# Kernel tuning notes

Measured on AMD Instinct MI355X. Metric: run time of the kernel, lower is better.

Reference implementation:

```python
import jax, jax.numpy as jnp
import numpy as np

N_QUBITS = 8
DEPTH = 3


def _apply_1q(state, U, q):
    # state: (2,)*n complex, apply 2x2 unitary U on qubit axis q
    state = jnp.moveaxis(state, q, -1)
    state = state @ U.T
    return jnp.moveaxis(state, -1, q)


def _ry(state, theta, q):
    h = theta * 0.5
    c, s = jnp.cos(h), jnp.sin(h)
    U = jnp.stack([jnp.stack([c, -s]), jnp.stack([s, c])]).astype(jnp.complex64)
    return _apply_1q(state, U, q)


def _rz(state, theta, q):
    h = theta * 0.5
    d = jnp.stack([jnp.exp(-1j * h), jnp.exp(1j * h)]).astype(jnp.complex64)
    state = jnp.moveaxis(state, q, -1) * d
    return jnp.moveaxis(state, -1, q)


def _cx(state, c, t):
    # CNOT with control c, target t: flip target amplitudes where control=1
    state = jnp.moveaxis(state, (c, t), (-2, -1))
    s0 = state[..., 0, :]
    s1 = state[..., 1, ::-1]
    state = jnp.stack([s0, s1], axis=-2)
    return jnp.moveaxis(state, (-2, -1), (c, t))


def _simulate(angles, qparams):
    # Single-sample circuit: RY angle encoding, then DEPTH layers of (RZ,RY) per
    # qubit + CX ring. Returns <Z_0> (Hamiltonian 'Z' + 'I'*(n-1)).
    state = jnp.zeros((2,) * N_QUBITS, jnp.complex64).at[(0,) * N_QUBITS].set(1.0)
    for q in range(N_QUBITS):
        state = _ry(state, angles[q], q)
    idx = 0
    for _ in range(DEPTH):
        for q in range(N_QUBITS):
            state = _rz(state, qparams[idx], q); idx += 1
            state = _ry(state, qparams[idx], q); idx += 1
        for i in range(N_QUBITS):
            state = _cx(state, i, (i + 1) % N_QUBITS)
    probs = jnp.abs(state) ** 2
    return probs[0].sum() - probs[1].sum()


def setup_inputs() -> dict:
    key = jax.random.key(0)
    ks = jax.random.split(key, 6)
    B, F, H = 16384, 16, 256
    nq = 2 * N_QUBITS * DEPTH  # 48 variational params
    return {
        "x": jax.random.normal(ks[0], (B, F), jnp.float32),
        "enc_w1": jax.random.normal(ks[1], (H, F), jnp.float32) / np.sqrt(F).astype(np.float32),
        "enc_b1": jnp.zeros((H,), jnp.float32),
        "enc_w2": jax.random.normal(ks[2], (N_QUBITS, H), jnp.float32) / np.sqrt(H).astype(np.float32),
        "enc_b2": jnp.zeros((N_QUBITS,), jnp.float32),
        "qparams": jax.random.normal(ks[3], (nq,), jnp.float32) * 0.1,
        "dec_w1": jax.random.normal(ks[4], (H, 1), jnp.float32),
        "dec_b1": jnp.zeros((H,), jnp.float32),
        "dec_w2": jax.random.normal(ks[5], (1, H), jnp.float32) / np.sqrt(H).astype(np.float32),
        "dec_b2": jnp.zeros((1,), jnp.float32),
    }


def reference(x, enc_w1, enc_b1, enc_w2, enc_b2, qparams, dec_w1, dec_b1, dec_w2, dec_b2):
    # encoder: Linear -> ReLU -> Linear -> Tanh, scaled by pi (angle encoding)
    h = jax.nn.relu(x @ enc_w1.T + enc_b1)
    angles = jnp.tanh(h @ enc_w2.T + enc_b2) * jnp.pi  # (B, n_qubits)
    # vectorized quantum state-vector simulation over the batch
    expvals = jax.vmap(_simulate, in_axes=(0, None))(angles, qparams)  # (B,)
    q = expvals[:, None]  # (B, 1)
    # decoder: Linear(1->H) -> ReLU -> Linear(H->1) -> Sigmoid
    d = jax.nn.relu(q @ dec_w1.T + dec_b1)
    return jax.nn.sigmoid(d @ dec_w2.T + dec_b2)
```

## Files before the change

### kernel.cpp

```cpp
#include <hip/hip_runtime.h>
#include <math.h>

#define NQ 8
#define DEPTH 3
#define FDIM 16
#define HDIM 256
#define WAVES_PER_BLOCK 4
#define THREADS (WAVES_PER_BLOCK * 64)
#define NGATE (NQ * DEPTH)
#define PI_F 3.14159265358979323846f

template<int CTRL>
__device__ __forceinline__ float dpp1(float v) {
    return __int_as_float(__builtin_amdgcn_update_dpp(
        0, __float_as_int(v), CTRL, 0xF, 0xF, true));
}

template<int M4>
__device__ __forceinline__ float shuf4(float v) {
    if constexpr (M4 == 0)  return v;
    else if constexpr (M4 == 1)  return dpp1<0xB1>(v);
    else if constexpr (M4 == 2)  return dpp1<0x4E>(v);
    else if constexpr (M4 == 3)  return dpp1<0x1B>(v);
    else if constexpr (M4 == 4)  return dpp1<0x1B>(dpp1<0x141>(v));
    else if constexpr (M4 == 5)  return dpp1<0x4E>(dpp1<0x141>(v));
    else if constexpr (M4 == 6)  return dpp1<0xB1>(dpp1<0x141>(v));
    else if constexpr (M4 == 7)  return dpp1<0x141>(v);
    else if constexpr (M4 == 8)  return dpp1<0x128>(v);
    else if constexpr (M4 == 9)  return dpp1<0xB1>(dpp1<0x128>(v));
    else if constexpr (M4 == 10) return dpp1<0x4E>(dpp1<0x128>(v));
    else if constexpr (M4 == 11) return dpp1<0x1B>(dpp1<0x128>(v));
    else if constexpr (M4 == 12) return dpp1<0x1B>(dpp1<0x140>(v));
    else if constexpr (M4 == 13) return dpp1<0x4E>(dpp1<0x140>(v));
    else if constexpr (M4 == 14) return dpp1<0xB1>(dpp1<0x140>(v));
    else                         return dpp1<0x140>(v);
}

template<int ML>
__device__ __forceinline__ float shuf(float v, int lane) {
    if constexpr (ML == 0) {
        return v;
    } else if constexpr (ML >= 32) {
        int addr = (lane ^ ML) << 2;
        return __int_as_float(__builtin_amdgcn_ds_bpermute(addr, __float_as_int(v)));
    } else if constexpr (ML >= 16) {
        return __int_as_float(__builtin_amdgcn_ds_swizzle(
            __float_as_int(v), (ML << 10) | 0x1F));
    } else {
        return shuf4<ML>(v);
    }
}

__device__ __forceinline__ float px16(float v, int lane) {
#if __has_builtin(__builtin_amdgcn_permlane16_swap)
    auto r = __builtin_amdgcn_permlane16_swap(__float_as_int(v), __float_as_int(v), false, false);
    return __int_as_float((lane & 16) ? r[0] : r[1]);
#else
    return __shfl_xor(v, 16, 64);
#endif
}
__device__ __forceinline__ float px32(float v, int lane) {
#if __has_builtin(__builtin_amdgcn_permlane32_swap)
    auto r = __builtin_amdgcn_permlane32_swap(__float_as_int(v), __float_as_int(v), false, false);
    return __int_as_float((lane & 32) ? r[0] : r[1]);
#else
    return __shfl_xor(v, 32, 64);
#endif
}

__device__ __forceinline__ float wred(float v, int lane) {
    v += shuf4<1>(v);
    v += shuf4<2>(v);
    v += shuf4<4>(v);
    v += shuf4<8>(v);
    v += px16(v, lane);
    v += px32(v, lane);
    return v;
}

__device__ __forceinline__ float fast_tanh(float y) {
    float ex = __expf(2.f * y);
    return 1.f - 2.f * __builtin_amdgcn_rcpf(ex + 1.f);
}

template<int M, int R>
__device__ __forceinline__ void gate2(float (&sr)[4], float (&si)[4],
                                      float cz, float szv, float cy, float sy,
                                      int lane) {
    constexpr int ML = M & 63, MH = (M >> 6) & 3;
    constexpr int RL = R & 63, RH = (R >> 6) & 3;
    bool p0;
    if constexpr (RL == 0)                 p0 = false;
    else if constexpr ((RL & (RL-1)) == 0) p0 = (lane & RL) != 0;
    else                                   p0 = (__popc(lane & RL) & 1) != 0;
    float sgz = p0 ? szv : -szv;
    float sgy = p0 ? sy  : -sy;
#pragma unroll
    for (int hi = 0; hi < 4; hi++) {
        const bool f = (__builtin_popcount(hi & RH) & 1) != 0;
        float z = f ? -sgz : sgz;
        float nr = fmaf(sr[hi], cz, -(si[hi] * z));
        float ni = fmaf(si[hi], cz,  (sr[hi] * z));
        sr[hi] = nr; si[hi] = ni;
    }
    float pr[4], pi[4];
#pragma unroll
    for (int hi = 0; hi < 4; hi++) {
        pr[hi] = shuf<ML>(sr[hi ^ MH], lane);
        pi[hi] = shuf<ML>(si[hi ^ MH], lane);
    }
#pragma unroll
    for (int hi = 0; hi < 4; hi++) {
        const bool f = (__builtin_popcount(hi & RH) & 1) != 0;
        float yv = f ? -sgy : sgy;
        sr[hi] = fmaf(yv, pr[hi], cy * sr[hi]);
        si[hi] = fmaf(yv, pi[hi], cy * si[hi]);
    }
}

__global__ __launch_bounds__(THREADS) void hqcl_kernel(
    const float* __restrict__ x,
    const float* __restrict__ w1,
    const float* __restrict__ b1,
    const float* __restrict__ w2,
    const float* __restrict__ b2,
    const float* __restrict__ qp,
    const float* __restrict__ dw1,
    const float* __restrict__ db1,
    const float* __restrict__ dw2,
    const float* __restrict__ db2,
    float* __restrict__ out, int B)
{
    __shared__ float4 sG4[NGATE];

    const int t = threadIdx.x;
    if (t < 2 * NGATE) {
        float s, c;
        __sincosf(qp[t] * 0.5f, &s, &c);
        float* p = (float*)&sG4[t >> 1] + 2 * (t & 1);
        p[0] = c; p[1] = s;
    }
    __syncthreads();

    const int lane = t & 63;
    const int row  = blockIdx.x * WAVES_PER_BLOCK + (t >> 6);
    if (row >= B) return;

    const float4* xp = (const float4*)(x + row * FDIM);
    float4 x0 = xp[0], x1 = xp[1], x2 = xp[2], x3 = xp[3];

    float hreg[4];
#pragma unroll
    for (int m = 0; m < 4; m++) {
        int j = lane + 64 * m;
        const float4* wp = (const float4*)(w1 + j * FDIM);
        float4 wa = wp[0], wb = wp[1], wc = wp[2], wd = wp[3];
        float acc = b1[j];
        acc = fmaf(x0.x, wa.x, acc); acc = fmaf(x0.y, wa.y, acc);
        acc = fmaf(x0.z, wa.z, acc); acc = fmaf(x0.w, wa.w, acc);
        acc = fmaf(x1.x, wb.x, acc); acc = fmaf(x1.y, wb.y, acc);
        acc = fmaf(x1.z, wb.z, acc); acc = fmaf(x1.w, wb.w, acc);
        acc = fmaf(x2.x, wc.x, acc); acc = fmaf(x2.y, wc.y, acc);
        acc = fmaf(x2.z, wc.z, acc); acc = fmaf(x2.w, wc.w, acc);
        acc = fmaf(x3.x, wd.x, acc); acc = fmaf(x3.y, wd.y, acc);
        acc = fmaf(x3.z, wd.z, acc); acc = fmaf(x3.w, wd.w, acc);
        hreg[m] = fmaxf(acc, 0.f);
    }

    float c0[NQ], s0[NQ];
#pragma unroll
    for (int q = 0; q < NQ; q++) {
        float a = 0.f;
#pragma unroll
        for (int m = 0; m < 4; m++)
            a = fmaf(hreg[m], w2[q * HDIM + lane + 64 * m], a);
        a = wred(a, lane);
        float ang = fast_tanh(a + b2[q]) * PI_F;
        __sincosf(ang * 0.5f, &s0[q], &c0[q]);
    }

    float pl = 1.f;
#pragma unroll
    for (int b = 0; b < 6; b++) {
        int q = 7 - b;
        pl *= ((lane >> b) & 1) ? s0[q] : c0[q];
    }
    float sr[4], si[4];
    sr[0] = pl * c0[1] * c0[0];
    sr[1] = pl * s0[1] * c0[0];
    sr[2] = pl * c0[1] * s0[0];
    sr[3] = pl * s0[1] * s0[0];
#pragma unroll
    for (int hi = 0; hi < 4; hi++) si[hi] = 0.f;

#define GATE(L, Q, MM, RR) { float4 g4 = sG4[(L)*8 + (Q)]; \
        gate2<MM, RR>(sr, si, g4.x, g4.y, g4.z, g4.w, lane); }
    GATE(0,0,0x80,0x80) GATE(0,1,0x40,0x40) GATE(0,2,0x20,0x20) GATE(0,3,0x10,0x10)
    GATE(0,4,0x08,0x08) GATE(0,5,0x04,0x04) GATE(0,6,0x02,0x02) GATE(0,7,0x01,0x01)
    GATE(1,0,0xC0,0x7F) GATE(1,1,0x60,0xC0) GATE(1,2,0x30,0xE0) GATE(1,3,0x18,0xF0)
    GATE(1,4,0x0C,0xF8) GATE(1,5,0x06,0xFC) GATE(1,6,0x03,0xFE) GATE(1,7,0xC1,0xFF)
    GATE(2,0,0xA0,0xD5) GATE(2,1,0x50,0xBF) GATE(2,2,0x28,0x5F) GATE(2,3,0x14,0xAF)
    GATE(2,4,0x0A,0x57) GATE(2,5,0x05,0xAB) GATE(2,6,0xC2,0x55) GATE(2,7,0x61,0xAA)
#undef GATE

    float m0 = sr[0]*sr[0] + si[0]*si[0] + sr[2]*sr[2] + si[2]*si[2];
    float m1 = sr[1]*sr[1] + si[1]*si[1] + sr[3]*sr[3] + si[3]*si[3];
    bool pb = (__popc(lane & 0x0C) & 1) != 0;
    float e = pb ? (m1 - m0) : (m0 - m1);
    e = wred(e, lane);

    float acc = 0.f;
#pragma unroll
    for (int m = 0; m < 4; m++) {
        int j = lane + 64 * m;
        float d = fmaxf(fmaf(e, dw1[j], db1[j]), 0.f);
        acc = fmaf(d, dw2[j], acc);
    }
    acc = wred(acc, lane);
    if (lane == 0) out[row] = 1.f / (1.f + __expf(-(acc + db2[0])));
}

extern "C" void kernel_launch(void* const* d_in, const int* in_sizes, int n_in,
                              void* d_out, int out_size, void* d_ws, size_t ws_size,
                              hipStream_t stream) {
    const float* x   = (const float*)d_in[0];
    const float* w1  = (const float*)d_in[1];
    const float* b1  = (const float*)d_in[2];
    const float* w2  = (const float*)d_in[3];
    const float* b2  = (const float*)d_in[4];
    const float* qp  = (const float*)d_in[5];
    const float* dw1 = (const float*)d_in[6];
    const float* db1 = (const float*)d_in[7];
    const float* dw2 = (const float*)d_in[8];
    const float* db2 = (const float*)d_in[9];
    float* out = (float*)d_out;

    const int B = in_sizes[0] / FDIM;
    const int grid = (B + WAVES_PER_BLOCK - 1) / WAVES_PER_BLOCK;
    hqcl_kernel<<<grid, THREADS, 0, stream>>>(x, w1, b1, w2, b2, qp, dw1, db1, dw2, db2, out, B);
}
```

Baseline: 42.86 us.

## Simulate four samples per wave with 16-lane state groups and fused RZ·RY gates

Each wave now handles four batch rows. The encoder still runs per row in a loop, and the angles go through LDS. The quantum simulation then packs four samples into one wave, 16 lanes each with 16 amplitudes per lane, so all lane shuffles are cheap DPP ops instead of ds_swizzle/bpermute. The RZ and RY gates are precombined into one fused 2x2 complex update using products of their sin/cos, and the decoder runs four rows at once. The cost is higher register pressure (32 state floats), a serial encoder loop, and an extra block barrier.

```diff
diff --git a/kernel.cpp b/kernel.cpp
--- a/kernel.cpp
+++ b/kernel.cpp
@@ -6,9 +6,9 @@
 #define FDIM 16
 #define HDIM 256
 #define WAVES_PER_BLOCK 4
-#define THREADS (WAVES_PER_BLOCK * 64)
+#define THREADS 256
+#define ROWS_PER_BLOCK 16
 #define NGATE (NQ * DEPTH)
-#define PI_F 3.14159265358979323846f
 
 template<int CTRL>
 __device__ __forceinline__ float dpp1(float v) {
@@ -17,7 +17,7 @@
 }
 
 template<int M4>
-__device__ __forceinline__ float shuf4(float v) {
+__device__ __forceinline__ float dppx(float v) {
     if constexpr (M4 == 0)  return v;
     else if constexpr (M4 == 1)  return dpp1<0xB1>(v);
     else if constexpr (M4 == 2)  return dpp1<0x4E>(v);
@@ -36,22 +36,7 @@
     else                         return dpp1<0x140>(v);
 }
 
-template<int ML>
-__device__ __forceinline__ float shuf(float v, int lane) {
-    if constexpr (ML == 0) {
-        return v;
-    } else if constexpr (ML >= 32) {
-        int addr = (lane ^ ML) << 2;
-        return __int_as_float(__builtin_amdgcn_ds_bpermute(addr, __float_as_int(v)));
-    } else if constexpr (ML >= 16) {
-        return __int_as_float(__builtin_amdgcn_ds_swizzle(
-            __float_as_int(v), (ML << 10) | 0x1F));
-    } else {
-        return shuf4<ML>(v);
-    }
-}
-
-__device__ __forceinline__ float px16(float v, int lane) {
+__device__ __forceinline__ float px16v(float v, int lane) {
 #if __has_builtin(__builtin_amdgcn_permlane16_swap)
     auto r = __builtin_amdgcn_permlane16_swap(__float_as_int(v), __float_as_int(v), false, false);
     return __int_as_float((lane & 16) ? r[0] : r[1]);
@@ -59,7 +44,7 @@
     return __shfl_xor(v, 16, 64);
 #endif
 }
-__device__ __forceinline__ float px32(float v, int lane) {
+__device__ __forceinline__ float px32v(float v, int lane) {
 #if __has_builtin(__builtin_amdgcn_permlane32_swap)
     auto r = __builtin_amdgcn_permlane32_swap(__float_as_int(v), __float_as_int(v), false, false);
     return __int_as_float((lane & 32) ? r[0] : r[1]);
@@ -69,12 +54,26 @@
 }
 
 __device__ __forceinline__ float wred(float v, int lane) {
-    v += shuf4<1>(v);
-    v += shuf4<2>(v);
-    v += shuf4<4>(v);
-    v += shuf4<8>(v);
-    v += px16(v, lane);
-    v += px32(v, lane);
+    v += dppx<1>(v);
+    v += dppx<2>(v);
+    v += dppx<4>(v);
+    v += dppx<8>(v);
+#if __has_builtin(__builtin_amdgcn_permlane16_swap)
+    {
+        auto r = __builtin_amdgcn_permlane16_swap(__float_as_int(v), __float_as_int(v), false, false);
+        v = __int_as_float(r[0]) + __int_as_float(r[1]);
+    }
+#else
+    v += __shfl_xor(v, 16, 64);
+#endif
+#if __has_builtin(__builtin_amdgcn_permlane32_swap)
+    {
+        auto r = __builtin_amdgcn_permlane32_swap(__float_as_int(v), __float_as_int(v), false, false);
+        v = __int_as_float(r[0]) + __int_as_float(r[1]);
+    }
+#else
+    v += __shfl_xor(v, 32, 64);
+#endif
     return v;
 }
 
@@ -84,37 +83,52 @@
 }
 
 template<int M, int R>
-__device__ __forceinline__ void gate2(float (&sr)[4], float (&si)[4],
-                                      float cz, float szv, float cy, float sy,
-                                      int lane) {
-    constexpr int ML = M & 63, MH = (M >> 6) & 3;
-    constexpr int RL = R & 63, RH = (R >> 6) & 3;
+__device__ __forceinline__ void gateq(float (&kr)[16], float (&ki)[16],
+                                      float a0, float a1, float b0, float b1,
+                                      int g) {
+    constexpr int MH = (M >> 4) & 15, ML = M & 15;
+    constexpr int RH = (R >> 4) & 15, RL = R & 15;
     bool p0;
     if constexpr (RL == 0)                 p0 = false;
-    else if constexpr ((RL & (RL-1)) == 0) p0 = (lane & RL) != 0;
-    else                                   p0 = (__popc(lane & RL) & 1) != 0;
-    float sgz = p0 ? szv : -szv;
-    float sgy = p0 ? sy  : -sy;
-#pragma unroll
-    for (int hi = 0; hi < 4; hi++) {
-        const bool f = (__builtin_popcount(hi & RH) & 1) != 0;
-        float z = f ? -sgz : sgz;
-        float nr = fmaf(sr[hi], cz, -(si[hi] * z));
-        float ni = fmaf(si[hi], cz,  (sr[hi] * z));
-        sr[hi] = nr; si[hi] = ni;
-    }
-    float pr[4], pi[4];
-#pragma unroll
-    for (int hi = 0; hi < 4; hi++) {
-        pr[hi] = shuf<ML>(sr[hi ^ MH], lane);
-        pi[hi] = shuf<ML>(si[hi ^ MH], lane);
-    }
-#pragma unroll
-    for (int hi = 0; hi < 4; hi++) {
-        const bool f = (__builtin_popcount(hi & RH) & 1) != 0;
-        float yv = f ? -sgy : sgy;
-        sr[hi] = fmaf(yv, pr[hi], cy * sr[hi]);
-        si[hi] = fmaf(yv, pi[hi], cy * si[hi]);
+    else if constexpr ((RL & (RL-1)) == 0) p0 = (g & RL) != 0;
+    else                                   p0 = (__popc(g & RL) & 1) != 0;
+    float ea1 = p0 ? a1 : -a1;
+    float eb0 = p0 ? b0 : -b0;
+
+    if constexpr (MH == 0) {
+#pragma unroll
+        for (int k = 0; k < 16; k++) {
+            float pr = dppx<ML>(kr[k]);
+            float pi = dppx<ML>(ki[k]);
+            const bool f = (__builtin_popcount(k & RH) & 1) != 0;
+            float za1 = f ? -ea1 : ea1;
+            float zb0 = f ? -eb0 : eb0;
+            float lr = fmaf(-za1, ki[k], a0 * kr[k]);
+            float li = fmaf( za1, kr[k], a0 * ki[k]);
+            kr[k] = fmaf( b1, pi, fmaf(zb0, pr, lr));
+            ki[k] = fmaf(-b1, pr, fmaf(zb0, pi, li));
+        }
+    } else {
+        constexpr int HB = (MH & 8) ? 8 : (MH & 4) ? 4 : (MH & 2) ? 2 : 1;
+#pragma unroll
+        for (int k = 0; k < 16; k++) {
+            if (k & HB) continue;
+            const int k2 = k ^ MH;
+            float pr1 = dppx<ML>(kr[k2]), pi1 = dppx<ML>(ki[k2]);
+            float pr2 = dppx<ML>(kr[k]),  pi2 = dppx<ML>(ki[k]);
+            const bool f1 = (__builtin_popcount(k  & RH) & 1) != 0;
+            const bool f2 = (__builtin_popcount(k2 & RH) & 1) != 0;
+            float za1a = f1 ? -ea1 : ea1, zb0a = f1 ? -eb0 : eb0;
+            float za1b = f2 ? -ea1 : ea1, zb0b = f2 ? -eb0 : eb0;
+            float lra = fmaf(-za1a, ki[k],  a0 * kr[k]);
+            float lia = fmaf( za1a, kr[k],  a0 * ki[k]);
+            float lrb = fmaf(-za1b, ki[k2], a0 * kr[k2]);
+            float lib = fmaf( za1b, kr[k2], a0 * ki[k2]);
+            kr[k]  = fmaf( b1, pi1, fmaf(zb0a, pr1, lra));
+            ki[k]  = fmaf(-b1, pr1, fmaf(zb0a, pi1, lia));
+            kr[k2] = fmaf( b1, pi2, fmaf(zb0b, pr2, lrb));
+            ki[k2] = fmaf(-b1, pr2, fmaf(zb0b, pi2, lib));
+        }
     }
 }
 
@@ -132,69 +146,88 @@
     float* __restrict__ out, int B)
 {
     __shared__ float4 sG4[NGATE];
+    __shared__ float  lds_u[ROWS_PER_BLOCK * NQ];
 
     const int t = threadIdx.x;
-    if (t < 2 * NGATE) {
-        float s, c;
-        __sincosf(qp[t] * 0.5f, &s, &c);
-        float* p = (float*)&sG4[t >> 1] + 2 * (t & 1);
-        p[0] = c; p[1] = s;
+    if (t < NGATE) {
+        float cz, sz, cy, sy;
+        __sincosf(qp[2 * t] * 0.5f,     &sz, &cz);
+        __sincosf(qp[2 * t + 1] * 0.5f, &sy, &cy);
+        sG4[t] = make_float4(cz * cy, sz * cy, cz * sy, sz * sy);
+    }
+
+    const int wave = t >> 6;
+    const int lane = t & 63;
+    const int rowbase = blockIdx.x * ROWS_PER_BLOCK + wave * 4;
+
+#pragma unroll 1
+    for (int rr = 0; rr < 4; rr++) {
+        const int row = rowbase + rr;
+        if (row >= B) break;
+        const float4* xp = (const float4*)(x + row * FDIM);
+        float4 x0 = xp[0], x1 = xp[1], x2 = xp[2], x3 = xp[3];
+
+        float hreg[4];
+#pragma unroll
+        for (int m = 0; m < 4; m++) {
+            int j = lane + 64 * m;
+            const float4* wp = (const float4*)(w1 + j * FDIM);
+            float4 wa = wp[0], wb = wp[1], wc = wp[2], wd = wp[3];
+            float acc = b1[j];
+            acc = fmaf(x0.x, wa.x, acc); acc = fmaf(x0.y, wa.y, acc);
+            acc = fmaf(x0.z, wa.z, acc); acc = fmaf(x0.w, wa.w, acc);
+            acc = fmaf(x1.x, wb.x, acc); acc = fmaf(x1.y, wb.y, acc);
+            acc = fmaf(x1.z, wb.z, acc); acc = fmaf(x1.w, wb.w, acc);
+            acc = fmaf(x2.x, wc.x, acc); acc = fmaf(x2.y, wc.y, acc);
+            acc = fmaf(x2.z, wc.z, acc); acc = fmaf(x2.w, wc.w, acc);
+            acc = fmaf(x3.x, wd.x, acc); acc = fmaf(x3.y, wd.y, acc);
+            acc = fmaf(x3.z, wd.z, acc); acc = fmaf(x3.w, wd.w, acc);
+            hreg[m] = fmaxf(acc, 0.f);
+        }
+
+        float myu = 0.f;
+#pragma unroll
+        for (int q = 0; q < NQ; q++) {
+            float a = 0.f;
+#pragma unroll
+            for (int m = 0; m < 4; m++)
+                a = fmaf(hreg[m], w2[q * HDIM + lane + 64 * m], a);
+            a = wred(a, lane);
+            float u = 0.25f * fast_tanh(a + b2[q]);
+            if (lane == q) myu = u;
+        }
+        if (lane < NQ) lds_u[(wave * 4 + rr) * NQ + lane] = myu;
     }
     __syncthreads();
 
-    const int lane = t & 63;
-    const int row  = blockIdx.x * WAVES_PER_BLOCK + (t >> 6);
-    if (row >= B) return;
-
-    const float4* xp = (const float4*)(x + row * FDIM);
-    float4 x0 = xp[0], x1 = xp[1], x2 = xp[2], x3 = xp[3];
-
-    float hreg[4];
-#pragma unroll
-    for (int m = 0; m < 4; m++) {
-        int j = lane + 64 * m;
-        const float4* wp = (const float4*)(w1 + j * FDIM);
-        float4 wa = wp[0], wb = wp[1], wc = wp[2], wd = wp[3];
-        float acc = b1[j];
-        acc = fmaf(x0.x, wa.x, acc); acc = fmaf(x0.y, wa.y, acc);
-        acc = fmaf(x0.z, wa.z, acc); acc = fmaf(x0.w, wa.w, acc);
-        acc = fmaf(x1.x, wb.x, acc); acc = fmaf(x1.y, wb.y, acc);
-        acc = fmaf(x1.z, wb.z, acc); acc = fmaf(x1.w, wb.w, acc);
-        acc = fmaf(x2.x, wc.x, acc); acc = fmaf(x2.y, wc.y, acc);
-        acc = fmaf(x2.z, wc.z, acc); acc = fmaf(x2.w, wc.w, acc);
-        acc = fmaf(x3.x, wd.x, acc); acc = fmaf(x3.y, wd.y, acc);
-        acc = fmaf(x3.z, wd.z, acc); acc = fmaf(x3.w, wd.w, acc);
-        hreg[m] = fmaxf(acc, 0.f);
-    }
-
-    float c0[NQ], s0[NQ];
-#pragma unroll
-    for (int q = 0; q < NQ; q++) {
-        float a = 0.f;
-#pragma unroll
-        for (int m = 0; m < 4; m++)
-            a = fmaf(hreg[m], w2[q * HDIM + lane + 64 * m], a);
-        a = wred(a, lane);
-        float ang = fast_tanh(a + b2[q]) * PI_F;
-        __sincosf(ang * 0.5f, &s0[q], &c0[q]);
-    }
-
-    float pl = 1.f;
-#pragma unroll
-    for (int b = 0; b < 6; b++) {
-        int q = 7 - b;
-        pl *= ((lane >> b) & 1) ? s0[q] : c0[q];
-    }
-    float sr[4], si[4];
-    sr[0] = pl * c0[1] * c0[0];
-    sr[1] = pl * s0[1] * c0[0];
-    sr[2] = pl * c0[1] * s0[0];
-    sr[3] = pl * s0[1] * s0[0];
-#pragma unroll
-    for (int hi = 0; hi < 4; hi++) si[hi] = 0.f;
+    const int g = lane & 15;
+    const float* up = lds_u + ((wave << 2) | (lane >> 4)) * NQ;
+    float4 uA = *(const float4*)(up);
+    float4 uB = *(const float4*)(up + 4);
+
+    float uu[8] = {uA.x, uA.y, uA.z, uA.w, uB.x, uB.y, uB.z, uB.w};
+    float sv[8], cv[8];
+#pragma unroll
+    for (int q = 0; q < 8; q++) {
+        asm("v_sin_f32 %0, %1" : "=v"(sv[q]) : "v"(uu[q]));
+        asm("v_cos_f32 %0, %1" : "=v"(cv[q]) : "v"(uu[q]));
+    }
+    float plg = ((g >> 3) & 1 ? sv[4] : cv[4]);
+    plg *= ((g >> 2) & 1 ? sv[5] : cv[5]);
+    plg *= ((g >> 1) & 1 ? sv[6] : cv[6]);
+    plg *= ((g      ) & 1 ? sv[7] : cv[7]);
+    float q01[4] = {cv[0]*cv[1], cv[0]*sv[1], sv[0]*cv[1], sv[0]*sv[1]};
+    float q23[4] = {cv[2]*cv[3], cv[2]*sv[3], sv[2]*cv[3], sv[2]*sv[3]};
+
+    float kr[16], ki[16];
+#pragma unroll
+    for (int k = 0; k < 16; k++) {
+        kr[k] = plg * q01[k >> 2] * q23[k & 3];
+        ki[k] = 0.f;
+    }
 
 #define GATE(L, Q, MM, RR) { float4 g4 = sG4[(L)*8 + (Q)]; \
-        gate2<MM, RR>(sr, si, g4.x, g4.y, g4.z, g4.w, lane); }
+        gateq<MM, RR>(kr, ki, g4.x, g4.y, g4.z, g4.w, g); }
     GATE(0,0,0x80,0x80) GATE(0,1,0x40,0x40) GATE(0,2,0x20,0x20) GATE(0,3,0x10,0x10)
     GATE(0,4,0x08,0x08) GATE(0,5,0x04,0x04) GATE(0,6,0x02,0x02) GATE(0,7,0x01,0x01)
     GATE(1,0,0xC0,0x7F) GATE(1,1,0x60,0xC0) GATE(1,2,0x30,0xE0) GATE(1,3,0x18,0xF0)
@@ -203,21 +236,52 @@
     GATE(2,4,0x0A,0x57) GATE(2,5,0x05,0xAB) GATE(2,6,0xC2,0x55) GATE(2,7,0x61,0xAA)
 #undef GATE
 
-    float m0 = sr[0]*sr[0] + si[0]*si[0] + sr[2]*sr[2] + si[2]*si[2];
-    float m1 = sr[1]*sr[1] + si[1]*si[1] + sr[3]*sr[3] + si[3]*si[3];
-    bool pb = (__popc(lane & 0x0C) & 1) != 0;
-    float e = pb ? (m1 - m0) : (m0 - m1);
-    e = wred(e, lane);
-
-    float acc = 0.f;
+    float tp = 0.f, tn = 0.f;
+#pragma unroll
+    for (int k = 0; k < 16; k++) {
+        float m = fmaf(kr[k], kr[k], ki[k] * ki[k]);
+        if ((k >> 2) & 1) tn += m; else tp += m;
+    }
+    float tt = tp - tn;
+    bool pg = (__popc(g & 0x0C) & 1) != 0;
+    float e = pg ? -tt : tt;
+    e += dppx<1>(e);
+    e += dppx<2>(e);
+    e += dppx<4>(e);
+    e += dppx<8>(e);
+
+    float eown = e;
+    float ex16 = px16v(e, lane);
+    float ex32 = px32v(e, lane);
+    float ex48 = px32v(ex16, lane);
+    bool s0b = (lane >> 4) & 1;
+    bool s1b = (lane >> 5) & 1;
+    float e0 = s1b ? (s0b ? ex48 : ex32) : (s0b ? ex16 : eown);
+    float e1 = s1b ? (s0b ? ex32 : ex48) : (s0b ? eown : ex16);
+    float e2 = s1b ? (s0b ? ex16 : eown) : (s0b ? ex48 : ex32);
+    float e3 = s1b ? (s0b ? eown : ex16) : (s0b ? ex32 : ex48);
+
+    float a0c = 0.f, a1c = 0.f, a2c = 0.f, a3c = 0.f;
 #pragma unroll
     for (int m = 0; m < 4; m++) {
         int j = lane + 64 * m;
-        float d = fmaxf(fmaf(e, dw1[j], db1[j]), 0.f);
-        acc = fmaf(d, dw2[j], acc);
-    }
-    acc = wred(acc, lane);
-    if (lane == 0) out[row] = 1.f / (1.f + __expf(-(acc + db2[0])));
+        float w1v = dw1[j], bv = db1[j], w2v = dw2[j];
+        a0c = fmaf(fmaxf(fmaf(e0, w1v, bv), 0.f), w2v, a0c);
+        a1c = fmaf(fmaxf(fmaf(e1, w1v, bv), 0.f), w2v, a1c);
+        a2c = fmaf(fmaxf(fmaf(e2, w1v, bv), 0.f), w2v, a2c);
+        a3c = fmaf(fmaxf(fmaf(e3, w1v, bv), 0.f), w2v, a3c);
+    }
+    a0c = wred(a0c, lane);
+    a1c = wred(a1c, lane);
+    a2c = wred(a2c, lane);
+    a3c = wred(a3c, lane);
+
+    if (lane < 4) {
+        float av = (lane == 0) ? a0c : (lane == 1) ? a1c : (lane == 2) ? a2c : a3c;
+        int orow = rowbase + lane;
+        if (orow < B)
+            out[orow] = 1.f / (1.f + __expf(-(av + db2[0])));
+    }
 }
 
 extern "C" void kernel_launch(void* const* d_in, const int* in_sizes, int n_in,
@@ -236,6 +300,6 @@
     float* out = (float*)d_out;
 
     const int B = in_sizes[0] / FDIM;
-    const int grid = (B + WAVES_PER_BLOCK - 1) / WAVES_PER_BLOCK;
+    const int grid = (B + ROWS_PER_BLOCK - 1) / ROWS_PER_BLOCK;
     hqcl_kernel<<<grid, THREADS, 0, stream>>>(x, w1, b1, w2, b2, qp, dw1, db1, dw2, db2, out, B);
 }
```

Measured after the change: 53.98 us. 1.26x slower.
